# Optimization experiments

Measured on AMD Instinct MI355X. Metric: run time of the kernel, lower is better.

## Reference

```python
import jax, jax.numpy as jnp
import numpy as np

B, S, INPUT_DIM = 8, 512, 64
D_MODEL, NUM_LAYERS, OUTPUT_DIM = 512, 4, 10
D_INNER, D_STATE, D_CONV, DT_RANK = 2 * D_MODEL, 16, 4, 32
GRID_SIZE, SPLINE_K = 5, 3
N_COEFF = GRID_SIZE + SPLINE_K  # 8
_H = 2.0 / GRID_SIZE
GRID = jnp.linspace(-1.0 - SPLINE_K * _H, 1.0 + SPLINE_K * _H, GRID_SIZE + 2 * SPLINE_K + 1)


def b_splines(x):
    # x: (..., in) -> (..., in, N_COEFF) via Cox-de Boor recursion on fixed GRID
    x = x[..., None]
    b = ((x >= GRID[:-1]) & (x < GRID[1:])).astype(x.dtype)
    for p in range(1, SPLINE_K + 1):
        left = (x - GRID[:-(p + 1)]) / (GRID[p:-1] - GRID[:-(p + 1)])
        right = (GRID[p + 1:] - x) / (GRID[p + 1:] - GRID[1:-p])
        b = left * b[..., :-1] + right * b[..., 1:]
    return b


def kan(x, base_w, spline_w):
    # efficient-KAN: silu base path + per-edge spline path
    return jax.nn.silu(x) @ base_w.T + jnp.einsum('...ik,oik->...o', b_splines(x), spline_w)


def layernorm(x, g, b):
    m = jnp.mean(x, -1, keepdims=True)
    v = jnp.var(x, -1, keepdims=True)
    return (x - m) / jnp.sqrt(v + 1e-5) * g + b


def liquid_proj(x, Win, Wrec, b, tau):
    # liquid time-constant RNN: h' = (tanh(Wx + Uh + b) - h) / tau
    pre = x @ Win  # (B,S,H)
    tau_pos = jax.nn.softplus(tau) + 0.1
    def step(h, p):
        act = jnp.tanh(p + h @ Wrec + b)
        h = h + (act - h) / tau_pos
        return h, h
    h0 = jnp.zeros((x.shape[0], Win.shape[1]), x.dtype)
    hT, hs = jax.lax.scan(step, h0, pre.transpose(1, 0, 2))
    return hs.transpose(1, 0, 2), hT


def mamba_block(x, in_proj_w, conv_w, conv_b, x_proj_w, dt_proj_w, dt_proj_b, A_log, Dp, out_proj_w):
    Bb, Ss, _ = x.shape
    xz = x @ in_proj_w.T                       # (B,S,2*di)
    xm, z = jnp.split(xz, 2, axis=-1)
    # causal depthwise conv1d with kernel D_CONV
    xp = jnp.pad(xm, ((0, 0), (D_CONV - 1, 0), (0, 0)))
    xm = sum(xp[:, k:k + Ss, :] * conv_w[:, k] for k in range(D_CONV)) + conv_b
    xm = jax.nn.silu(xm)
    x_dbl = xm @ x_proj_w.T                    # (B,S,dt_rank+2n)
    dt, Bc, Cc = jnp.split(x_dbl, [DT_RANK, DT_RANK + D_STATE], axis=-1)
    dt = jax.nn.softplus(dt @ dt_proj_w.T + dt_proj_b)   # (B,S,di)
    A = -jnp.exp(A_log)                        # (di,n)
    dA = jnp.exp(dt[..., None] * A)            # (B,S,di,n)
    dBu = dt[..., None] * Bc[:, :, None, :] * xm[..., None]
    def step(h, inp):
        a, bu, c = inp
        h = a * h + bu
        return h, jnp.einsum('bdn,bn->bd', h, c)
    h0 = jnp.zeros((Bb, D_INNER, D_STATE), x.dtype)
    _, ys = jax.lax.scan(step, h0, (dA.transpose(1, 0, 2, 3), dBu.transpose(1, 0, 2, 3), Cc.transpose(1, 0, 2)))
    y = ys.transpose(1, 0, 2) + Dp * xm
    y = y * jax.nn.silu(z)
    return y @ out_proj_w.T


def forward(x, lq_Win, lq_Wrec, lq_b, lq_tau, ln_g, ln_b, in_proj_w, conv_w, conv_b,
            x_proj_w, dt_proj_w, dt_proj_b, A_log, Dp, out_proj_w,
            kan_base_w, kan_spline_w, fn_g, fn_b, cls_base_w, cls_spline_w):
    x, _ = liquid_proj(x, lq_Win, lq_Wrec, lq_b, lq_tau)
    for l in range(NUM_LAYERS):
        residual = x
        xn = layernorm(x, ln_g[l], ln_b[l])
        xm = mamba_block(xn, in_proj_w[l], conv_w[l], conv_b[l], x_proj_w[l],
                         dt_proj_w[l], dt_proj_b[l], A_log[l], Dp[l], out_proj_w[l])
        x = residual + kan(xm, kan_base_w[l], kan_spline_w[l])
    x = layernorm(x, fn_g, fn_b)
    return kan(x.mean(axis=1), cls_base_w, cls_spline_w)


def setup_inputs():
    key = jax.random.key(0)
    ks = jax.random.split(key, 12)
    n = lambda k, shape, s: jax.random.normal(k, shape, jnp.float32) * s
    return {
        "x": n(ks[0], (B, S, INPUT_DIM), 1.0),
        "lq_Win": n(ks[1], (INPUT_DIM, D_MODEL), INPUT_DIM ** -0.5),
        "lq_Wrec": n(ks[2], (D_MODEL, D_MODEL), D_MODEL ** -0.5),
        "lq_b": jnp.zeros((D_MODEL,), jnp.float32),
        "lq_tau": jnp.ones((D_MODEL,), jnp.float32),
        "ln_g": jnp.ones((NUM_LAYERS, D_MODEL), jnp.float32),
        "ln_b": jnp.zeros((NUM_LAYERS, D_MODEL), jnp.float32),
        "in_proj_w": n(ks[3], (NUM_LAYERS, 2 * D_INNER, D_MODEL), D_MODEL ** -0.5),
        "conv_w": n(ks[4], (NUM_LAYERS, D_INNER, D_CONV), D_CONV ** -0.5),
        "conv_b": jnp.zeros((NUM_LAYERS, D_INNER), jnp.float32),
        "x_proj_w": n(ks[5], (NUM_LAYERS, DT_RANK + 2 * D_STATE, D_INNER), D_INNER ** -0.5),
        "dt_proj_w": n(ks[6], (NUM_LAYERS, D_INNER, DT_RANK), DT_RANK ** -0.5),
        "dt_proj_b": jnp.full((NUM_LAYERS, D_INNER), float(np.log(np.expm1(0.01))), jnp.float32),
        "A_log": jnp.log(jnp.broadcast_to(jnp.arange(1, D_STATE + 1, dtype=jnp.float32), (NUM_LAYERS, D_INNER, D_STATE))),
        "Dp": jnp.ones((NUM_LAYERS, D_INNER), jnp.float32),
        "out_proj_w": n(ks[7], (NUM_LAYERS, D_MODEL, D_INNER), D_INNER ** -0.5),
        "kan_base_w": n(ks[8], (NUM_LAYERS, D_MODEL, D_MODEL), D_MODEL ** -0.5),
        "kan_spline_w": n(ks[9], (NUM_LAYERS, D_MODEL, D_MODEL, N_COEFF), 0.1 * D_MODEL ** -0.5),
        "fn_g": jnp.ones((D_MODEL,), jnp.float32),
        "fn_b": jnp.zeros((D_MODEL,), jnp.float32),
        "cls_base_w": n(ks[10], (OUTPUT_DIM, D_MODEL), D_MODEL ** -0.5),
        "cls_spline_w": n(ks[11], (OUTPUT_DIM, D_MODEL, N_COEFF), 0.1 * D_MODEL ** -0.5),
    }


def reference(x, lq_Win, lq_Wrec, lq_b, lq_tau, ln_g, ln_b, in_proj_w, conv_w, conv_b,
              x_proj_w, dt_proj_w, dt_proj_b, A_log, Dp, out_proj_w,
              kan_base_w, kan_spline_w, fn_g, fn_b, cls_base_w, cls_spline_w):
    return forward(x, lq_Win, lq_Wrec, lq_b, lq_tau, ln_g, ln_b, in_proj_w, conv_w, conv_b,
                   x_proj_w, dt_proj_w, dt_proj_b, A_log, Dp, out_proj_w,
                   kan_base_w, kan_spline_w, fn_g, fn_b, cls_base_w, cls_spline_w)
```

## Files before the change

### kernel.cpp

```cpp
#include <hip/hip_runtime.h>
#include <hip/hip_bf16.h>
#include <cmath>

#define DEV __device__ __forceinline__

constexpr int B_ = 8, S_ = 512, IN_ = 64, D_ = 512, L_ = 4;
constexpr int DI_ = 1024, DCONV_ = 4, DTR_ = 32;
constexpr int ROWS = B_ * S_;

constexpr size_t MB = 1ull << 20;
constexpr size_t OFF_X    = 0;
constexpr size_t OFF_XN   = OFF_X   + 8*MB;
constexpr size_t OFF_XZ   = OFF_XN  + 8*MB;
constexpr size_t OFF_XM   = OFF_XZ  + 32*MB;
constexpr size_t OFF_DT   = OFF_XM  + 16*MB;
constexpr size_t OFF_XDBL = OFF_DT  + 16*MB;
constexpr size_t OFF_YG   = OFF_XDBL+ 1*MB;
constexpr size_t OFF_MO   = OFF_YG  + 16*MB;
constexpr size_t OFF_WINT = OFF_MO  + 8*MB;
constexpr size_t OFF_MEAN = OFF_WINT+ 128*1024;
constexpr size_t OFF_HBUF = OFF_MEAN+ 16*1024;
constexpr size_t OFF_FLG  = OFF_HBUF+ 32*1024;
constexpr size_t OFF_BASIS= OFF_XZ;

DEV float siluf(float x){ return x / (1.f + __expf(-x)); }
DEV float softplusf(float x){ return fmaxf(x, 0.f) + log1pf(__expf(-fabsf(x))); }
DEV unsigned short f2h(float f){ return __builtin_bit_cast(unsigned short, (_Float16)f); }

DEV void bspline8(float x, float* bb){
  const float h = 0.4f, g0 = -2.2f;
  float b0[11];
#pragma unroll
  for (int j = 0; j < 11; ++j){
    float gj  = g0 + h * j;
    float gj1 = g0 + h * (j + 1);
    b0[j] = (x >= gj && x < gj1) ? 1.f : 0.f;
  }
#pragma unroll
  for (int p = 1; p <= 3; ++p){
    float inv = 1.f / (h * p);
#pragma unroll
    for (int j = 0; j + p < 11; ++j){
      float gj  = g0 + h * j;
      float gip = g0 + h * (j + p + 1);
      b0[j] = (x - gj) * inv * b0[j] + (gip - x) * inv * b0[j + 1];
    }
  }
#pragma unroll
  for (int c = 0; c < 8; ++c) bb[c] = b0[c];
}

template<bool SILU_A, int EPI>
__global__ __launch_bounds__(256)
void gemm_nt(const float* __restrict__ A, int lda,
             const float* __restrict__ W, int ldw,
             float* __restrict__ C, int ldc,
             const float* __restrict__ bias, int K)
{
  __shared__ float As[16][68];
  __shared__ float Ws[16][68];
  const int tid = threadIdx.x;
  const int m0 = blockIdx.y * 64, n0 = blockIdx.x * 64;
  const int lr = tid >> 2, lc = (tid & 3) * 4;
  const float* Ap = A + (size_t)(m0 + lr) * lda + lc;
  const float* Wp = W + (size_t)(n0 + lr) * ldw + lc;
  const int tx = tid & 15, ty = tid >> 4;
  float acc[4][4] = {};
  for (int k0 = 0; k0 < K; k0 += 16){
    float4 a = *(const float4*)(Ap + k0);
    float4 w = *(const float4*)(Wp + k0);
    if (SILU_A){ a.x = siluf(a.x); a.y = siluf(a.y); a.z = siluf(a.z); a.w = siluf(a.w); }
    __syncthreads();
    As[lc+0][lr] = a.x; As[lc+1][lr] = a.y; As[lc+2][lr] = a.z; As[lc+3][lr] = a.w;
    Ws[lc+0][lr] = w.x; Ws[lc+1][lr] = w.y; Ws[lc+2][lr] = w.z; Ws[lc+3][lr] = w.w;
    __syncthreads();
#pragma unroll
    for (int k = 0; k < 16; ++k){
      float4 av = *(const float4*)&As[k][ty*4];
      float4 wv = *(const float4*)&Ws[k][tx*4];
      acc[0][0] += av.x*wv.x; acc[0][1] += av.x*wv.y; acc[0][2] += av.x*wv.z; acc[0][3] += av.x*wv.w;
      acc[1][0] += av.y*wv.x; acc[1][1] += av.y*wv.y; acc[1][2] += av.y*wv.z; acc[1][3] += av.y*wv.w;
      acc[2][0] += av.z*wv.x; acc[2][1] += av.z*wv.y; acc[2][2] += av.z*wv.z; acc[2][3] += av.z*wv.w;
      acc[3][0] += av.w*wv.x; acc[3][1] += av.w*wv.y; acc[3][2] += av.w*wv.z; acc[3][3] += av.w*wv.w;
    }
  }
#pragma unroll
  for (int i = 0; i < 4; ++i){
    float* Crow = C + (size_t)(m0 + ty*4 + i) * ldc + n0 + tx*4;
    float4 r = {acc[i][0], acc[i][1], acc[i][2], acc[i][3]};
    if (EPI == 1){
      float4 c0 = *(const float4*)Crow;
      r.x += c0.x; r.y += c0.y; r.z += c0.z; r.w += c0.w;
    } else if (EPI == 2){
      const float* bp = bias + n0 + tx*4;
      r.x = softplusf(r.x + bp[0]); r.y = softplusf(r.y + bp[1]);
      r.z = softplusf(r.z + bp[2]); r.w = softplusf(r.w + bp[3]);
    }
    *(float4*)Crow = r;
  }
}

typedef _Float16 half8 __attribute__((ext_vector_type(8)));
typedef float f32x4 __attribute__((ext_vector_type(4)));

DEV int pk2(float a, float b){ return (int)((unsigned)f2h(a) | ((unsigned)f2h(b) << 16)); }

template<bool SILU_A, bool ACCUM>
__global__ __launch_bounds__(256)
void gemm_f16(const float* __restrict__ A, int lda,
              const float* __restrict__ W, int ldw,
              float* __restrict__ C, int ldc, int K)
{
  __shared__ unsigned short As[128*40];
  __shared__ unsigned short Bs[128*40];
  const int tid = threadIdx.x;
  const int m0 = blockIdx.y * 128, n0 = blockIdx.x * 128;
  const int wid = tid >> 6, lane = tid & 63;
  const int wm = (wid & 1) * 64, wn = (wid >> 1) * 64;
  const int fr = lane & 15, fk = lane >> 4;
  const int sr = tid >> 1, sh = tid & 1;

  f32x4 acc[4][4];
#pragma unroll
  for (int i = 0; i < 4; ++i)
#pragma unroll
    for (int j = 0; j < 4; ++j)
#pragma unroll
      for (int r = 0; r < 4; ++r) acc[i][j][r] = 0.f;

  for (int k0 = 0; k0 < K; k0 += 32){
    const float* ag = A + (size_t)(m0 + sr) * lda + k0 + sh*16;
    float4 a0 = *(const float4*)ag,     a1 = *(const float4*)(ag+4);
    float4 a2 = *(const float4*)(ag+8), a3 = *(const float4*)(ag+12);
    if (SILU_A){
      a0.x=siluf(a0.x); a0.y=siluf(a0.y); a0.z=siluf(a0.z); a0.w=siluf(a0.w);
      a1.x=siluf(a1.x); a1.y=siluf(a1.y); a1.z=siluf(a1.z); a1.w=siluf(a1.w);
      a2.x=siluf(a2.x); a2.y=siluf(a2.y); a2.z=siluf(a2.z); a2.w=siluf(a2.w);
      a3.x=siluf(a3.x); a3.y=siluf(a3.y); a3.z=siluf(a3.z); a3.w=siluf(a3.w);
    }
    int4 av0 = { pk2(a0.x,a0.y), pk2(a0.z,a0.w), pk2(a1.x,a1.y), pk2(a1.z,a1.w) };
    int4 av1 = { pk2(a2.x,a2.y), pk2(a2.z,a2.w), pk2(a3.x,a3.y), pk2(a3.z,a3.w) };
    const float* wg = W + (size_t)(n0 + sr) * ldw + k0 + sh*16;
    float4 w0 = *(const float4*)wg,     w1 = *(const float4*)(wg+4);
    float4 w2 = *(const float4*)(wg+8), w3 = *(const float4*)(wg+12);
    int4 bv0 = { pk2(w0.x,w0.y), pk2(w0.z,w0.w), pk2(w1.x,w1.y), pk2(w1.z,w1.w) };
    int4 bv1 = { pk2(w2.x,w2.y), pk2(w2.z,w2.w), pk2(w3.x,w3.y), pk2(w3.z,w3.w) };
    __syncthreads();
    *(int4*)&As[sr*40 + sh*16]     = av0;
    *(int4*)&As[sr*40 + sh*16 + 8] = av1;
    *(int4*)&Bs[sr*40 + sh*16]     = bv0;
    *(int4*)&Bs[sr*40 + sh*16 + 8] = bv1;
    __syncthreads();
    half8 a[4], b[4];
#pragma unroll
    for (int i = 0; i < 4; ++i) a[i] = *(const half8*)&As[(wm + i*16 + fr)*40 + fk*8];
#pragma unroll
    for (int j = 0; j < 4; ++j) b[j] = *(const half8*)&Bs[(wn + j*16 + fr)*40 + fk*8];
#pragma unroll
    for (int i = 0; i < 4; ++i)
#pragma unroll
      for (int j = 0; j < 4; ++j)
        acc[i][j] = __builtin_amdgcn_mfma_f32_16x16x32_f16(a[i], b[j], acc[i][j], 0, 0, 0);
  }
#pragma unroll
  for (int i = 0; i < 4; ++i)
#pragma unroll
    for (int j = 0; j < 4; ++j){
      int col = n0 + wn + j*16 + fr;
#pragma unroll
      for (int r = 0; r < 4; ++r){
        int row = m0 + wm + i*16 + fk*4 + r;
        if (ACCUM) C[(size_t)row * ldc + col] += acc[i][j][r];
        else       C[(size_t)row * ldc + col]  = acc[i][j][r];
      }
    }
}

__global__ __launch_bounds__(256)
void gemm_spline_f16(const unsigned short* __restrict__ A,
                     const float* __restrict__ W,
                     float* __restrict__ C)
{
  __shared__ unsigned short As[128*40];
  __shared__ unsigned short Bs[128*40];
  const int tid = threadIdx.x;
  const int m0 = blockIdx.y * 128, n0 = blockIdx.x * 128;
  const int wid = tid >> 6, lane = tid & 63;
  const int wm = (wid & 1) * 64, wn = (wid >> 1) * 64;
  const int fr = lane & 15, fk = lane >> 4;
  const int sr = tid >> 1, sh = tid & 1;

  f32x4 acc[4][4];
#pragma unroll
  for (int i = 0; i < 4; ++i)
#pragma unroll
    for (int j = 0; j < 4; ++j)
#pragma unroll
      for (int r = 0; r < 4; ++r) acc[i][j][r] = 0.f;

  for (int k0 = 0; k0 < 4096; k0 += 32){
    const unsigned short* ag = A + (size_t)(m0 + sr) * 4096 + k0 + sh*16;
    int4 a0 = *(const int4*)ag;
    int4 a1 = *(const int4*)(ag + 8);
    const float* wg = W + (size_t)(n0 + sr) * 4096 + k0 + sh*16;
    float4 w0 = *(const float4*)wg,     w1 = *(const float4*)(wg+4);
    float4 w2 = *(const float4*)(wg+8), w3 = *(const float4*)(wg+12);
    int4 b0 = { pk2(w0.x,w0.y), pk2(w0.z,w0.w), pk2(w1.x,w1.y), pk2(w1.z,w1.w) };
    int4 b1 = { pk2(w2.x,w2.y), pk2(w2.z,w2.w), pk2(w3.x,w3.y), pk2(w3.z,w3.w) };
    __syncthreads();
    *(int4*)&As[sr*40 + sh*16]     = a0;
    *(int4*)&As[sr*40 + sh*16 + 8] = a1;
    *(int4*)&Bs[sr*40 + sh*16]     = b0;
    *(int4*)&Bs[sr*40 + sh*16 + 8] = b1;
    __syncthreads();
    half8 a[4], b[4];
#pragma unroll
    for (int i = 0; i < 4; ++i) a[i] = *(const half8*)&As[(wm + i*16 + fr)*40 + fk*8];
#pragma unroll
    for (int j = 0; j < 4; ++j) b[j] = *(const half8*)&Bs[(wn + j*16 + fr)*40 + fk*8];
#pragma unroll
    for (int i = 0; i < 4; ++i)
#pragma unroll
      for (int j = 0; j < 4; ++j)
        acc[i][j] = __builtin_amdgcn_mfma_f32_16x16x32_f16(a[i], b[j], acc[i][j], 0, 0, 0);
  }
#pragma unroll
  for (int i = 0; i < 4; ++i)
#pragma unroll
    for (int j = 0; j < 4; ++j){
      int col = n0 + wn + j*16 + fr;
#pragma unroll
      for (int r = 0; r < 4; ++r){
        int row = m0 + wm + i*16 + fk*4 + r;
        C[(size_t)row * 512 + col] += acc[i][j][r];
      }
    }
}

__global__ __launch_bounds__(256)
void transpose_win(const float* __restrict__ Win, float* __restrict__ WinT)
{
  int idx = blockIdx.x * 256 + threadIdx.x;
  int n = idx >> 6, k = idx & 63;
  WinT[idx] = Win[(size_t)k * 512 + n];
}

__global__ __launch_bounds__(512)
void liquid_scan3(const float* __restrict__ pre, const float* __restrict__ Wrec,
                  const float* __restrict__ bias, const float* __restrict__ tau,
                  float* __restrict__ xout, float* __restrict__ hbuf,
                  unsigned* __restrict__ flags)
{
  __shared__ float Wl[32800];
  __shared__ float hl[544];
  __shared__ float hnew[64];
  const int tid = threadIdx.x;
  const int bid = blockIdx.x;
  const int slice = bid >> 3, b = bid & 7;
  for (int idx = tid; idx < 512*16; idx += 512){
    int k = idx >> 4, c4 = (idx & 15) * 4;
    float4 w = *(const float4*)(Wrec + (size_t)k*512 + slice*64 + c4);
    *(float4*)&Wl[k*64 + c4 + (k>>6)*4] = w;
  }
  hl[tid + (tid>>6)*4] = 0.f;
  const int o = tid >> 3, kl = tid & 7;
  const int og = slice*64 + o;
  const float tauinv = 1.f / (softplusf(tau[og]) + 0.1f);
  const float bo = bias[og];
  float hold = 0.f;
  const float* preb = pre + (size_t)b * S_ * 512;
  float* xb = xout + (size_t)b * S_ * 512;
  float* hb0 = hbuf + (size_t)b * 512;
  unsigned* bflags = flags + b*8*16;
  unsigned* myflag = bflags + slice*16;
  const int kbase = kl * 64;
  const float* wp = &Wl[(size_t)kbase*64 + o + kl*4];
  __syncthreads();
  for (int t = 0; t < S_; ++t){
    float prev = (kl == 0) ? preb[(size_t)t*512 + og] : 0.f;
    float hreg[64];
#pragma unroll
    for (int j4 = 0; j4 < 16; ++j4)
      *(float4*)&hreg[j4*4] = *(const float4*)&hl[kbase + kl*4 + j4*4];
    float s = 0.f;
#pragma unroll
    for (int j = 0; j < 64; ++j)
      s += hreg[j] * wp[(size_t)j * 64];
    s += __shfl_xor(s, 1);
    s += __shfl_xor(s, 2);
    s += __shfl_xor(s, 4);
    if (kl == 0){
      float act = tanhf(s + prev + bo);
      hold += (act - hold) * tauinv;
      xb[(size_t)t*512 + og] = hold;
      hnew[o] = hold;
    }
    __syncthreads();
    if (tid < 64)
      __hip_atomic_store(hb0 + (t&1)*4096 + slice*64 + tid, hnew[tid],
                         __ATOMIC_RELAXED, __HIP_MEMORY_SCOPE_AGENT);
    if (tid == 0){
      asm volatile("s_waitcnt vmcnt(0)" ::: "memory");
      __hip_atomic_store(myflag, (unsigned)(t+1),
                         __ATOMIC_RELAXED, __HIP_MEMORY_SCOPE_AGENT);
    }
    if (tid < 8){
      while (__hip_atomic_load(bflags + tid*16, __ATOMIC_RELAXED,
                               __HIP_MEMORY_SCOPE_AGENT) < (unsigned)(t+1))
        __builtin_amdgcn_s_sleep(1);
    }
    __syncthreads();
    float hv = __hip_atomic_load(hb0 + (t&1)*4096 + tid,
                                 __ATOMIC_RELAXED, __HIP_MEMORY_SCOPE_AGENT);
    hl[tid + (tid>>6)*4] = hv;
    __syncthreads();
  }
}

__global__ __launch_bounds__(256)
void conv_silu(const float* __restrict__ xz, const float* __restrict__ cw,
               const float* __restrict__ cb, float* __restrict__ xm)
{
  int idx = blockIdx.x * 256 + threadIdx.x;
  int d = idx & 1023;
  int bs = idx >> 10;
  int t = bs & 511;
  const float* p = xz + (size_t)bs * 2048 + d;
  float4 w = *(const float4*)(cw + d*4);
  float acc = cb[d] + w.w * p[0];
  if (t >= 1) acc += w.z * p[-2048];
  if (t >= 2) acc += w.y * p[-2*2048];
  if (t >= 3) acc += w.x * p[-3*2048];
  xm[idx] = siluf(acc);
}

__global__ __launch_bounds__(256)
void mamba_scan(const float* __restrict__ dt, const float* __restrict__ xm,
                const float* __restrict__ xdbl, const float* __restrict__ xz,
                const float* __restrict__ A_log, const float* __restrict__ Dp,
                float* __restrict__ yg)
{
  const int tid = threadIdx.x;
  const int wave = tid >> 6, lane = tid & 63;
  const int half = lane >> 5, dl = lane & 31;
  const int d = blockIdx.x * 128 + wave * 32 + dl;
  const int b = blockIdx.y;
  float A[8];
  {
    float4 a0 = *(const float4*)(A_log + (size_t)d*16 + half*8);
    float4 a1 = *(const float4*)(A_log + (size_t)d*16 + half*8 + 4);
    A[0] = -__expf(a0.x); A[1] = -__expf(a0.y); A[2] = -__expf(a0.z); A[3] = -__expf(a0.w);
    A[4] = -__expf(a1.x); A[5] = -__expf(a1.y); A[6] = -__expf(a1.z); A[7] = -__expf(a1.w);
  }
  const float Dv = Dp[d];
  float h[8] = {0,0,0,0,0,0,0,0};
  const size_t rb = (size_t)b * S_;
  const float* dtp = dt + rb*1024 + d;
  const float* xmp = xm + rb*1024 + d;
  const float* zp  = xz + rb*2048 + 1024 + d;
  const float* bcp = xdbl + rb*64 + 32 + half*8;
  const float* ccp = xdbl + rb*64 + 48 + half*8;
  float* yp = yg + rb*1024 + d;
  for (int t = 0; t < S_; ++t){
    float dtv = dtp[(size_t)t*1024];
    float xv  = xmp[(size_t)t*1024];
    float4 b0 = *(const float4*)(bcp + (size_t)t*64);
    float4 b1 = *(const float4*)(bcp + (size_t)t*64 + 4);
    float4 c0 = *(const float4*)(ccp + (size_t)t*64);
    float4 c1 = *(const float4*)(ccp + (size_t)t*64 + 4);
    float Bv[8] = {b0.x,b0.y,b0.z,b0.w,b1.x,b1.y,b1.z,b1.w};
    float Cv[8] = {c0.x,c0.y,c0.z,c0.w,c1.x,c1.y,c1.z,c1.w};
    float cbu = dtv * xv;
    float y = 0.f;
#pragma unroll
    for (int n = 0; n < 8; ++n){
      float da = __expf(dtv * A[n]);
      h[n] = da * h[n] + cbu * Bv[n];
      y += h[n] * Cv[n];
    }
    y += __shfl_xor(y, 32);
    if (half == 0){
      float zv = zp[(size_t)t*2048];
      yp[(size_t)t*1024] = (y + Dv * xv) * siluf(zv);
    }
  }
}

__global__ __launch_bounds__(256)
void layernorm_k(const float* __restrict__ x, const float* __restrict__ g,
                 const float* __restrict__ b, float* __restrict__ y)
{
  __shared__ float red[8];
  const int row = blockIdx.x, tid = threadIdx.x;
  const float* xr = x + (size_t)row * 512;
  float2 v = *(const float2*)(xr + tid*2);
  float s = v.x + v.y;
#pragma unroll
  for (int o = 32; o; o >>= 1) s += __shfl_xor(s, o);
  if ((tid & 63) == 0) red[tid >> 6] = s;
  __syncthreads();
  float mean = (red[0] + red[1] + red[2] + red[3]) * (1.f/512.f);
  float dx = v.x - mean, dy = v.y - mean;
  float q = dx*dx + dy*dy;
#pragma unroll
  for (int o = 32; o; o >>= 1) q += __shfl_xor(q, o);
  if ((tid & 63) == 0) red[4 + (tid >> 6)] = q;
  __syncthreads();
  float var = (red[4] + red[5] + red[6] + red[7]) * (1.f/512.f);
  float rstd = rsqrtf(var + 1e-5f);
  float2 gg = *(const float2*)(g + tid*2);
  float2 bb = *(const float2*)(b + tid*2);
  float2 o2;
  o2.x = dx*rstd*gg.x + bb.x;
  o2.y = dy*rstd*gg.y + bb.y;
  *(float2*)(y + (size_t)row*512 + tid*2) = o2;
}

__global__ __launch_bounds__(256)
void bspline_kernel(const float* __restrict__ xin, unsigned short* __restrict__ basis)
{
  int idx = blockIdx.x * 256 + threadIdx.x;
  float x = xin[idx];
  float bb[8];
  bspline8(x, bb);
  int4 v = { pk2(bb[0],bb[1]), pk2(bb[2],bb[3]), pk2(bb[4],bb[5]), pk2(bb[6],bb[7]) };
  *(int4*)(basis + (size_t)idx * 8) = v;
}

__global__ __launch_bounds__(512)
void mean_over_s(const float* __restrict__ x, float* __restrict__ out)
{
  int b = blockIdx.x, d = threadIdx.x;
  const float* p = x + (size_t)b*S_*512 + d;
  float s = 0.f;
  for (int t = 0; t < S_; ++t) s += p[(size_t)t*512];
  out[b*512 + d] = s * (1.f/512.f);
}

__global__ __launch_bounds__(64)
void cls_kan(const float* __restrict__ xmean, const float* __restrict__ bw,
             const float* __restrict__ sw, float* __restrict__ out)
{
  int o = blockIdx.x % 10, b = blockIdx.x / 10;
  int lane = threadIdx.x;
  float acc = 0.f;
  for (int i = lane; i < 512; i += 64){
    float xv = xmean[b*512 + i];
    acc += siluf(xv) * bw[o*512 + i];
    float bb[8]; bspline8(xv, bb);
    const float* sp = sw + ((size_t)(o*512 + i)) * 8;
#pragma unroll
    for (int c = 0; c < 8; ++c) acc += bb[c] * sp[c];
  }
#pragma unroll
  for (int off = 32; off; off >>= 1) acc += __shfl_xor(acc, off);
  if (lane == 0) out[b*10 + o] = acc;
}

extern "C" void kernel_launch(void* const* d_in, const int* in_sizes, int n_in,
                              void* d_out, int out_size, void* d_ws, size_t ws_size,
                              hipStream_t stream)
{
  const float* x_in    = (const float*)d_in[0];
  const float* lq_Win  = (const float*)d_in[1];
  const float* lq_Wrec = (const float*)d_in[2];
  const float* lq_b    = (const float*)d_in[3];
  const float* lq_tau  = (const float*)d_in[4];
  const float* ln_g    = (const float*)d_in[5];
  const float* ln_bi   = (const float*)d_in[6];
  const float* in_proj = (const float*)d_in[7];
  const float* conv_w  = (const float*)d_in[8];
  const float* conv_b  = (const float*)d_in[9];
  const float* x_proj  = (const float*)d_in[10];
  const float* dt_w    = (const float*)d_in[11];
  const float* dt_b    = (const float*)d_in[12];
  const float* A_log   = (const float*)d_in[13];
  const float* Dp      = (const float*)d_in[14];
  const float* out_w   = (const float*)d_in[15];
  const float* kb_w    = (const float*)d_in[16];
  const float* ks_w    = (const float*)d_in[17];
  const float* fn_g    = (const float*)d_in[18];
  const float* fn_b    = (const float*)d_in[19];
  const float* cb_w    = (const float*)d_in[20];
  const float* cs_w    = (const float*)d_in[21];
  float* out = (float*)d_out;

  char* ws = (char*)d_ws;
  float* xcur  = (float*)(ws + OFF_X);
  float* xn    = (float*)(ws + OFF_XN);
  float* xz    = (float*)(ws + OFF_XZ);
  float* xm    = (float*)(ws + OFF_XM);
  float* dtb   = (float*)(ws + OFF_DT);
  float* xdbl  = (float*)(ws + OFF_XDBL);
  float* yg    = (float*)(ws + OFF_YG);
  float* mo    = (float*)(ws + OFF_MO);
  float* wint  = (float*)(ws + OFF_WINT);
  float* xmean = (float*)(ws + OFF_MEAN);
  float* hbufp = (float*)(ws + OFF_HBUF);
  unsigned* flgp = (unsigned*)(ws + OFF_FLG);
  unsigned short* basis = (unsigned short*)(ws + OFF_BASIS);

  transpose_win<<<128, 256, 0, stream>>>(lq_Win, wint);
  gemm_nt<false,0><<<dim3(D_/64, ROWS/64), 256, 0, stream>>>(x_in, IN_, wint, IN_, xn, D_, nullptr, IN_);
  hipMemsetAsync(flgp, 0, 8*8*16*sizeof(unsigned), stream);
  liquid_scan3<<<64, 512, 0, stream>>>(xn, lq_Wrec, lq_b, lq_tau, xcur, hbufp, flgp);

  for (int l = 0; l < L_; ++l){
    layernorm_k<<<ROWS, 256, 0, stream>>>(xcur, ln_g + l*D_, ln_bi + l*D_, xn);
    gemm_f16<false,false><<<dim3(2048/128, 4096/128), 256, 0, stream>>>(
        xn, D_, in_proj + (size_t)l*2*DI_*D_, D_, xz, 2*DI_, D_);
    conv_silu<<<ROWS*DI_/256, 256, 0, stream>>>(xz, conv_w + l*DI_*DCONV_, conv_b + l*DI_, xm);
    gemm_nt<false,0><<<dim3(1, ROWS/64), 256, 0, stream>>>(
        xm, DI_, x_proj + (size_t)l*64*DI_, DI_, xdbl, 64, nullptr, DI_);
    gemm_nt<false,2><<<dim3(DI_/64, ROWS/64), 256, 0, stream>>>(
        xdbl, 64, dt_w + (size_t)l*DI_*DTR_, DTR_, dtb, DI_, dt_b + l*DI_, DTR_);
    mamba_scan<<<dim3(DI_/128, B_), 256, 0, stream>>>(
        dtb, xm, xdbl, xz, A_log + (size_t)l*DI_*16, Dp + l*DI_, yg);
    gemm_f16<false,false><<<dim3(512/128, 4096/128), 256, 0, stream>>>(
        yg, DI_, out_w + (size_t)l*D_*DI_, DI_, mo, D_, DI_);
    bspline_kernel<<<ROWS*D_/256, 256, 0, stream>>>(mo, basis);
    gemm_f16<true,true><<<dim3(512/128, 4096/128), 256, 0, stream>>>(
        mo, D_, kb_w + (size_t)l*D_*D_, D_, xcur, D_, D_);
    gemm_spline_f16<<<dim3(512/128, 4096/128), 256, 0, stream>>>(
        basis, ks_w + (size_t)l*D_*D_*8, xcur);
  }

  layernorm_k<<<ROWS, 256, 0, stream>>>(xcur, fn_g, fn_b, xn);
  mean_over_s<<<B_, 512, 0, stream>>>(xn, xmean);
  cls_kan<<<B_*10, 64, 0, stream>>>(xmean, cb_w, cs_w, out);
}
```

Baseline: 4.487 ms.

## Pre-convert weights to fp16, use MFMA for small GEMMs, retile scan and GEMMs

Adds a kernel that converts every layer's weights to fp16 once per call. All GEMMs, including x_proj and dt_proj, now read these fp16 weights and run through MFMA GEMM templates, with a new 128x64 tile variant that gives the N=512 GEMMs more blocks. Layernorm and the Mamba scan now write fp16 activations directly. The scan is reorganised so 8 lanes each hold 2 state elements per channel, which raises parallelism. In exchange there is an extra conversion pass and lower precision for the x_proj and dt_proj paths.

```diff
diff --git a/kernel.cpp b/kernel.cpp
--- a/kernel.cpp
+++ b/kernel.cpp
@@ -21,11 +21,24 @@
 constexpr size_t OFF_MEAN = OFF_WINT+ 128*1024;
 constexpr size_t OFF_HBUF = OFF_MEAN+ 16*1024;
 constexpr size_t OFF_FLG  = OFF_HBUF+ 32*1024;
+constexpr size_t OFF_W16  = OFF_FLG + 64*1024;
 constexpr size_t OFF_BASIS= OFF_XZ;
+
+constexpr size_t W_IP = 0;
+constexpr size_t W_OP = 1048576;
+constexpr size_t W_KB = 1572864;
+constexpr size_t W_KS = 1835008;
+constexpr size_t W_XP = 3932160;
+constexpr size_t W_DT = 3997696;
+constexpr size_t W_PER_LAYER = 4030464;
 
 DEV float siluf(float x){ return x / (1.f + __expf(-x)); }
 DEV float softplusf(float x){ return fmaxf(x, 0.f) + log1pf(__expf(-fabsf(x))); }
 DEV unsigned short f2h(float f){ return __builtin_bit_cast(unsigned short, (_Float16)f); }
+DEV int pk2(float a, float b){ return (int)((unsigned)f2h(a) | ((unsigned)f2h(b) << 16)); }
+
+typedef _Float16 half8 __attribute__((ext_vector_type(8)));
+typedef float f32x4 __attribute__((ext_vector_type(4)));
 
 DEV void bspline8(float x, float* bb){
   const float h = 0.4f, g0 = -2.2f;
@@ -48,6 +61,26 @@
   }
 #pragma unroll
   for (int c = 0; c < 8; ++c) bb[c] = b0[c];
+}
+
+__global__ __launch_bounds__(256)
+void conv_w16(const float* __restrict__ ip, const float* __restrict__ op,
+              const float* __restrict__ kb, const float* __restrict__ ks,
+              const float* __restrict__ xp, const float* __restrict__ dt,
+              unsigned short* __restrict__ w16)
+{
+  int blk = blockIdx.x, tid = threadIdx.x;
+  const float* src; size_t doff; int sb;
+  if      (blk < 512) { src = ip; doff = W_IP; sb = blk; }
+  else if (blk < 768) { src = op; doff = W_OP; sb = blk - 512; }
+  else if (blk < 896) { src = kb; doff = W_KB; sb = blk - 768; }
+  else if (blk < 1920){ src = ks; doff = W_KS; sb = blk - 896; }
+  else if (blk < 1952){ src = xp; doff = W_XP; sb = blk - 1920; }
+  else                { src = dt; doff = W_DT; sb = blk - 1952; }
+  size_t e = (size_t)sb * 2048 + tid * 8;
+  float4 a = *(const float4*)(src + e), b = *(const float4*)(src + e + 4);
+  int4 v = { pk2(a.x,a.y), pk2(a.z,a.w), pk2(b.x,b.y), pk2(b.z,b.w) };
+  *(int4*)&w16[doff + e] = v;
 }
 
 template<bool SILU_A, int EPI>
@@ -88,28 +121,17 @@
   for (int i = 0; i < 4; ++i){
     float* Crow = C + (size_t)(m0 + ty*4 + i) * ldc + n0 + tx*4;
     float4 r = {acc[i][0], acc[i][1], acc[i][2], acc[i][3]};
-    if (EPI == 1){
-      float4 c0 = *(const float4*)Crow;
-      r.x += c0.x; r.y += c0.y; r.z += c0.z; r.w += c0.w;
-    } else if (EPI == 2){
-      const float* bp = bias + n0 + tx*4;
-      r.x = softplusf(r.x + bp[0]); r.y = softplusf(r.y + bp[1]);
-      r.z = softplusf(r.z + bp[2]); r.w = softplusf(r.w + bp[3]);
-    }
     *(float4*)Crow = r;
   }
 }
 
-typedef _Float16 half8 __attribute__((ext_vector_type(8)));
-typedef float f32x4 __attribute__((ext_vector_type(4)));
-
-DEV int pk2(float a, float b){ return (int)((unsigned)f2h(a) | ((unsigned)f2h(b) << 16)); }
-
-template<bool SILU_A, bool ACCUM>
-__global__ __launch_bounds__(256)
-void gemm_f16(const float* __restrict__ A, int lda,
-              const float* __restrict__ W, int ldw,
-              float* __restrict__ C, int ldc, int K)
+
+template<int AMODE, int EPI>
+__global__ __launch_bounds__(256)
+void gemm_h128(const void* __restrict__ Av, int lda,
+               const unsigned short* __restrict__ W,
+               float* __restrict__ C, int ldc,
+               const float* __restrict__ bias, int K)
 {
   __shared__ unsigned short As[128*40];
   __shared__ unsigned short Bs[128*40];
@@ -129,22 +151,25 @@
       for (int r = 0; r < 4; ++r) acc[i][j][r] = 0.f;
 
   for (int k0 = 0; k0 < K; k0 += 32){
-    const float* ag = A + (size_t)(m0 + sr) * lda + k0 + sh*16;
-    float4 a0 = *(const float4*)ag,     a1 = *(const float4*)(ag+4);
-    float4 a2 = *(const float4*)(ag+8), a3 = *(const float4*)(ag+12);
-    if (SILU_A){
-      a0.x=siluf(a0.x); a0.y=siluf(a0.y); a0.z=siluf(a0.z); a0.w=siluf(a0.w);
-      a1.x=siluf(a1.x); a1.y=siluf(a1.y); a1.z=siluf(a1.z); a1.w=siluf(a1.w);
-      a2.x=siluf(a2.x); a2.y=siluf(a2.y); a2.z=siluf(a2.z); a2.w=siluf(a2.w);
-      a3.x=siluf(a3.x); a3.y=siluf(a3.y); a3.z=siluf(a3.z); a3.w=siluf(a3.w);
-    }
-    int4 av0 = { pk2(a0.x,a0.y), pk2(a0.z,a0.w), pk2(a1.x,a1.y), pk2(a1.z,a1.w) };
-    int4 av1 = { pk2(a2.x,a2.y), pk2(a2.z,a2.w), pk2(a3.x,a3.y), pk2(a3.z,a3.w) };
-    const float* wg = W + (size_t)(n0 + sr) * ldw + k0 + sh*16;
-    float4 w0 = *(const float4*)wg,     w1 = *(const float4*)(wg+4);
-    float4 w2 = *(const float4*)(wg+8), w3 = *(const float4*)(wg+12);
-    int4 bv0 = { pk2(w0.x,w0.y), pk2(w0.z,w0.w), pk2(w1.x,w1.y), pk2(w1.z,w1.w) };
-    int4 bv1 = { pk2(w2.x,w2.y), pk2(w2.z,w2.w), pk2(w3.x,w3.y), pk2(w3.z,w3.w) };
+    int4 av0, av1;
+    if (AMODE == 0){
+      const unsigned short* ag = (const unsigned short*)Av + (size_t)(m0 + sr) * lda + k0 + sh*16;
+      av0 = *(const int4*)ag; av1 = *(const int4*)(ag + 8);
+    } else {
+      const float* ag = (const float*)Av + (size_t)(m0 + sr) * lda + k0 + sh*16;
+      float4 a0 = *(const float4*)ag,     a1 = *(const float4*)(ag+4);
+      float4 a2 = *(const float4*)(ag+8), a3 = *(const float4*)(ag+12);
+      if (AMODE == 2){
+        a0.x=siluf(a0.x); a0.y=siluf(a0.y); a0.z=siluf(a0.z); a0.w=siluf(a0.w);
+        a1.x=siluf(a1.x); a1.y=siluf(a1.y); a1.z=siluf(a1.z); a1.w=siluf(a1.w);
+        a2.x=siluf(a2.x); a2.y=siluf(a2.y); a2.z=siluf(a2.z); a2.w=siluf(a2.w);
+        a3.x=siluf(a3.x); a3.y=siluf(a3.y); a3.z=siluf(a3.z); a3.w=siluf(a3.w);
+      }
+      av0 = (int4){ pk2(a0.x,a0.y), pk2(a0.z,a0.w), pk2(a1.x,a1.y), pk2(a1.z,a1.w) };
+      av1 = (int4){ pk2(a2.x,a2.y), pk2(a2.z,a2.w), pk2(a3.x,a3.y), pk2(a3.z,a3.w) };
+    }
+    const unsigned short* wg = W + (size_t)(n0 + sr) * K + k0 + sh*16;
+    int4 bv0 = *(const int4*)wg, bv1 = *(const int4*)(wg + 8);
     __syncthreads();
     *(int4*)&As[sr*40 + sh*16]     = av0;
     *(int4*)&As[sr*40 + sh*16 + 8] = av1;
@@ -170,69 +195,86 @@
 #pragma unroll
       for (int r = 0; r < 4; ++r){
         int row = m0 + wm + i*16 + fk*4 + r;
-        if (ACCUM) C[(size_t)row * ldc + col] += acc[i][j][r];
-        else       C[(size_t)row * ldc + col]  = acc[i][j][r];
+        float* cp = C + (size_t)row * ldc + col;
+        if (EPI == 0)      *cp = acc[i][j][r];
+        else if (EPI == 1) *cp += acc[i][j][r];
+        else               *cp = softplusf(acc[i][j][r] + bias[col]);
       }
     }
 }
 
-__global__ __launch_bounds__(256)
-void gemm_spline_f16(const unsigned short* __restrict__ A,
-                     const float* __restrict__ W,
-                     float* __restrict__ C)
+template<int AMODE, int EPI>
+__global__ __launch_bounds__(256)
+void gemm_h64(const void* __restrict__ Av, int lda,
+              const unsigned short* __restrict__ W,
+              float* __restrict__ C, int ldc,
+              const float* __restrict__ bias, int K)
 {
   __shared__ unsigned short As[128*40];
-  __shared__ unsigned short Bs[128*40];
+  __shared__ unsigned short Bs[64*40];
   const int tid = threadIdx.x;
-  const int m0 = blockIdx.y * 128, n0 = blockIdx.x * 128;
+  const int m0 = blockIdx.y * 128, n0 = blockIdx.x * 64;
   const int wid = tid >> 6, lane = tid & 63;
-  const int wm = (wid & 1) * 64, wn = (wid >> 1) * 64;
   const int fr = lane & 15, fk = lane >> 4;
   const int sr = tid >> 1, sh = tid & 1;
-
-  f32x4 acc[4][4];
-#pragma unroll
-  for (int i = 0; i < 4; ++i)
+  const int br = tid >> 2, bq = tid & 3;
+
+  f32x4 acc[2][4];
+#pragma unroll
+  for (int i = 0; i < 2; ++i)
 #pragma unroll
     for (int j = 0; j < 4; ++j)
 #pragma unroll
       for (int r = 0; r < 4; ++r) acc[i][j][r] = 0.f;
 
-  for (int k0 = 0; k0 < 4096; k0 += 32){
-    const unsigned short* ag = A + (size_t)(m0 + sr) * 4096 + k0 + sh*16;
-    int4 a0 = *(const int4*)ag;
-    int4 a1 = *(const int4*)(ag + 8);
-    const float* wg = W + (size_t)(n0 + sr) * 4096 + k0 + sh*16;
-    float4 w0 = *(const float4*)wg,     w1 = *(const float4*)(wg+4);
-    float4 w2 = *(const float4*)(wg+8), w3 = *(const float4*)(wg+12);
-    int4 b0 = { pk2(w0.x,w0.y), pk2(w0.z,w0.w), pk2(w1.x,w1.y), pk2(w1.z,w1.w) };
-    int4 b1 = { pk2(w2.x,w2.y), pk2(w2.z,w2.w), pk2(w3.x,w3.y), pk2(w3.z,w3.w) };
-    __syncthreads();
-    *(int4*)&As[sr*40 + sh*16]     = a0;
-    *(int4*)&As[sr*40 + sh*16 + 8] = a1;
-    *(int4*)&Bs[sr*40 + sh*16]     = b0;
-    *(int4*)&Bs[sr*40 + sh*16 + 8] = b1;
-    __syncthreads();
-    half8 a[4], b[4];
-#pragma unroll
-    for (int i = 0; i < 4; ++i) a[i] = *(const half8*)&As[(wm + i*16 + fr)*40 + fk*8];
-#pragma unroll
-    for (int j = 0; j < 4; ++j) b[j] = *(const half8*)&Bs[(wn + j*16 + fr)*40 + fk*8];
-#pragma unroll
-    for (int i = 0; i < 4; ++i)
+  for (int k0 = 0; k0 < K; k0 += 32){
+    int4 av0, av1;
+    if (AMODE == 0){
+      const unsigned short* ag = (const unsigned short*)Av + (size_t)(m0 + sr) * lda + k0 + sh*16;
+      av0 = *(const int4*)ag; av1 = *(const int4*)(ag + 8);
+    } else {
+      const float* ag = (const float*)Av + (size_t)(m0 + sr) * lda + k0 + sh*16;
+      float4 a0 = *(const float4*)ag,     a1 = *(const float4*)(ag+4);
+      float4 a2 = *(const float4*)(ag+8), a3 = *(const float4*)(ag+12);
+      if (AMODE == 2){
+        a0.x=siluf(a0.x); a0.y=siluf(a0.y); a0.z=siluf(a0.z); a0.w=siluf(a0.w);
+        a1.x=siluf(a1.x); a1.y=siluf(a1.y); a1.z=siluf(a1.z); a1.w=siluf(a1.w);
+        a2.x=siluf(a2.x); a2.y=siluf(a2.y); a2.z=siluf(a2.z); a2.w=siluf(a2.w);
+        a3.x=siluf(a3.x); a3.y=siluf(a3.y); a3.z=siluf(a3.z); a3.w=siluf(a3.w);
+      }
+      av0 = (int4){ pk2(a0.x,a0.y), pk2(a0.z,a0.w), pk2(a1.x,a1.y), pk2(a1.z,a1.w) };
+      av1 = (int4){ pk2(a2.x,a2.y), pk2(a2.z,a2.w), pk2(a3.x,a3.y), pk2(a3.z,a3.w) };
+    }
+    const unsigned short* wg = W + (size_t)(n0 + br) * K + k0 + bq*8;
+    int4 bv0 = *(const int4*)wg;
+    __syncthreads();
+    *(int4*)&As[sr*40 + sh*16]     = av0;
+    *(int4*)&As[sr*40 + sh*16 + 8] = av1;
+    *(int4*)&Bs[br*40 + bq*8]      = bv0;
+    __syncthreads();
+    half8 a[2], b[4];
+#pragma unroll
+    for (int i = 0; i < 2; ++i) a[i] = *(const half8*)&As[(wid*32 + i*16 + fr)*40 + fk*8];
+#pragma unroll
+    for (int j = 0; j < 4; ++j) b[j] = *(const half8*)&Bs[(j*16 + fr)*40 + fk*8];
+#pragma unroll
+    for (int i = 0; i < 2; ++i)
 #pragma unroll
       for (int j = 0; j < 4; ++j)
         acc[i][j] = __builtin_amdgcn_mfma_f32_16x16x32_f16(a[i], b[j], acc[i][j], 0, 0, 0);
   }
 #pragma unroll
-  for (int i = 0; i < 4; ++i)
+  for (int i = 0; i < 2; ++i)
 #pragma unroll
     for (int j = 0; j < 4; ++j){
-      int col = n0 + wn + j*16 + fr;
+      int col = n0 + j*16 + fr;
 #pragma unroll
       for (int r = 0; r < 4; ++r){
-        int row = m0 + wm + i*16 + fk*4 + r;
-        C[(size_t)row * 512 + col] += acc[i][j][r];
+        int row = m0 + wid*32 + i*16 + fk*4 + r;
+        float* cp = C + (size_t)row * ldc + col;
+        if (EPI == 0)      *cp = acc[i][j][r];
+        else if (EPI == 1) *cp += acc[i][j][r];
+        else               *cp = softplusf(acc[i][j][r] + bias[col]);
       }
     }
 }
@@ -335,60 +377,51 @@
 }
 
 __global__ __launch_bounds__(256)
-void mamba_scan(const float* __restrict__ dt, const float* __restrict__ xm,
-                const float* __restrict__ xdbl, const float* __restrict__ xz,
-                const float* __restrict__ A_log, const float* __restrict__ Dp,
-                float* __restrict__ yg)
+void mamba_scan2(const float* __restrict__ dt, const float* __restrict__ xm,
+                 const float* __restrict__ xdbl, const float* __restrict__ xz,
+                 const float* __restrict__ A_log, const float* __restrict__ Dp,
+                 unsigned short* __restrict__ yg)
 {
   const int tid = threadIdx.x;
   const int wave = tid >> 6, lane = tid & 63;
-  const int half = lane >> 5, dl = lane & 31;
-  const int d = blockIdx.x * 128 + wave * 32 + dl;
+  const int ch = lane >> 3, sub = lane & 7;
+  const int d = blockIdx.x * 32 + wave * 8 + ch;
   const int b = blockIdx.y;
-  float A[8];
-  {
-    float4 a0 = *(const float4*)(A_log + (size_t)d*16 + half*8);
-    float4 a1 = *(const float4*)(A_log + (size_t)d*16 + half*8 + 4);
-    A[0] = -__expf(a0.x); A[1] = -__expf(a0.y); A[2] = -__expf(a0.z); A[3] = -__expf(a0.w);
-    A[4] = -__expf(a1.x); A[5] = -__expf(a1.y); A[6] = -__expf(a1.z); A[7] = -__expf(a1.w);
-  }
+  float2 al = *(const float2*)(A_log + (size_t)d*16 + sub*2);
+  const float A0 = -__expf(al.x), A1 = -__expf(al.y);
   const float Dv = Dp[d];
-  float h[8] = {0,0,0,0,0,0,0,0};
+  float h0 = 0.f, h1 = 0.f;
   const size_t rb = (size_t)b * S_;
   const float* dtp = dt + rb*1024 + d;
   const float* xmp = xm + rb*1024 + d;
   const float* zp  = xz + rb*2048 + 1024 + d;
-  const float* bcp = xdbl + rb*64 + 32 + half*8;
-  const float* ccp = xdbl + rb*64 + 48 + half*8;
-  float* yp = yg + rb*1024 + d;
+  const float* bcp = xdbl + rb*64 + 32 + sub*2;
+  const float* ccp = xdbl + rb*64 + 48 + sub*2;
+  unsigned short* yp = yg + rb*1024 + d;
+#pragma unroll 2
   for (int t = 0; t < S_; ++t){
     float dtv = dtp[(size_t)t*1024];
     float xv  = xmp[(size_t)t*1024];
-    float4 b0 = *(const float4*)(bcp + (size_t)t*64);
-    float4 b1 = *(const float4*)(bcp + (size_t)t*64 + 4);
-    float4 c0 = *(const float4*)(ccp + (size_t)t*64);
-    float4 c1 = *(const float4*)(ccp + (size_t)t*64 + 4);
-    float Bv[8] = {b0.x,b0.y,b0.z,b0.w,b1.x,b1.y,b1.z,b1.w};
-    float Cv[8] = {c0.x,c0.y,c0.z,c0.w,c1.x,c1.y,c1.z,c1.w};
+    float2 B2 = *(const float2*)(bcp + (size_t)t*64);
+    float2 C2 = *(const float2*)(ccp + (size_t)t*64);
     float cbu = dtv * xv;
-    float y = 0.f;
-#pragma unroll
-    for (int n = 0; n < 8; ++n){
-      float da = __expf(dtv * A[n]);
-      h[n] = da * h[n] + cbu * Bv[n];
-      y += h[n] * Cv[n];
-    }
-    y += __shfl_xor(y, 32);
-    if (half == 0){
+    h0 = __expf(dtv * A0) * h0 + cbu * B2.x;
+    h1 = __expf(dtv * A1) * h1 + cbu * B2.y;
+    float y = h0 * C2.x + h1 * C2.y;
+    y += __shfl_xor(y, 1);
+    y += __shfl_xor(y, 2);
+    y += __shfl_xor(y, 4);
+    if (sub == 0){
       float zv = zp[(size_t)t*2048];
-      yp[(size_t)t*1024] = (y + Dv * xv) * siluf(zv);
-    }
-  }
-}
-
+      yp[(size_t)t*1024] = f2h((y + Dv * xv) * siluf(zv));
+    }
+  }
+}
+
+template<bool H>
 __global__ __launch_bounds__(256)
 void layernorm_k(const float* __restrict__ x, const float* __restrict__ g,
-                 const float* __restrict__ b, float* __restrict__ y)
+                 const float* __restrict__ b, void* __restrict__ y)
 {
   __shared__ float red[8];
   const int row = blockIdx.x, tid = threadIdx.x;
@@ -410,10 +443,15 @@
   float rstd = rsqrtf(var + 1e-5f);
   float2 gg = *(const float2*)(g + tid*2);
   float2 bb = *(const float2*)(b + tid*2);
-  float2 o2;
-  o2.x = dx*rstd*gg.x + bb.x;
-  o2.y = dy*rstd*gg.y + bb.y;
-  *(float2*)(y + (size_t)row*512 + tid*2) = o2;
+  float ox = dx*rstd*gg.x + bb.x;
+  float oy = dy*rstd*gg.y + bb.y;
+  if (H){
+    unsigned* yr = (unsigned*)y + (size_t)row*256 + tid;
+    *yr = (unsigned)f2h(ox) | ((unsigned)f2h(oy) << 16);
+  } else {
+    float2 o2 = {ox, oy};
+    *(float2*)((float*)y + (size_t)row*512 + tid*2) = o2;
+  }
 }
 
 __global__ __launch_bounds__(256)
@@ -487,45 +525,56 @@
 
   char* ws = (char*)d_ws;
   float* xcur  = (float*)(ws + OFF_X);
-  float* xn    = (float*)(ws + OFF_XN);
+  float* xn32  = (float*)(ws + OFF_XN);
+  unsigned short* xn16 = (unsigned short*)(ws + OFF_XN);
   float* xz    = (float*)(ws + OFF_XZ);
   float* xm    = (float*)(ws + OFF_XM);
   float* dtb   = (float*)(ws + OFF_DT);
   float* xdbl  = (float*)(ws + OFF_XDBL);
-  float* yg    = (float*)(ws + OFF_YG);
+  unsigned short* yg16 = (unsigned short*)(ws + OFF_YG);
   float* mo    = (float*)(ws + OFF_MO);
   float* wint  = (float*)(ws + OFF_WINT);
   float* xmean = (float*)(ws + OFF_MEAN);
   float* hbufp = (float*)(ws + OFF_HBUF);
   unsigned* flgp = (unsigned*)(ws + OFF_FLG);
+  unsigned short* w16 = (unsigned short*)(ws + OFF_W16);
   unsigned short* basis = (unsigned short*)(ws + OFF_BASIS);
 
   transpose_win<<<128, 256, 0, stream>>>(lq_Win, wint);
-  gemm_nt<false,0><<<dim3(D_/64, ROWS/64), 256, 0, stream>>>(x_in, IN_, wint, IN_, xn, D_, nullptr, IN_);
+  gemm_nt<false,0><<<dim3(D_/64, ROWS/64), 256, 0, stream>>>(x_in, IN_, wint, IN_, xn32, D_, nullptr, IN_);
   hipMemsetAsync(flgp, 0, 8*8*16*sizeof(unsigned), stream);
-  liquid_scan3<<<64, 512, 0, stream>>>(xn, lq_Wrec, lq_b, lq_tau, xcur, hbufp, flgp);
+  liquid_scan3<<<64, 512, 0, stream>>>(xn32, lq_Wrec, lq_b, lq_tau, xcur, hbufp, flgp);
 
   for (int l = 0; l < L_; ++l){
-    layernorm_k<<<ROWS, 256, 0, stream>>>(xcur, ln_g + l*D_, ln_bi + l*D_, xn);
-    gemm_f16<false,false><<<dim3(2048/128, 4096/128), 256, 0, stream>>>(
-        xn, D_, in_proj + (size_t)l*2*DI_*D_, D_, xz, 2*DI_, D_);
+    conv_w16<<<1968, 256, 0, stream>>>(
+        in_proj + (size_t)l*2*DI_*D_, out_w + (size_t)l*D_*DI_,
+        kb_w + (size_t)l*D_*D_, ks_w + (size_t)l*D_*D_*8,
+        x_proj + (size_t)l*64*DI_, dt_w + (size_t)l*DI_*DTR_,
+        w16 + (size_t)l*W_PER_LAYER);
+  }
+
+  for (int l = 0; l < L_; ++l){
+    const unsigned short* wl = w16 + (size_t)l*W_PER_LAYER;
+    layernorm_k<true><<<ROWS, 256, 0, stream>>>(xcur, ln_g + l*D_, ln_bi + l*D_, xn16);
+    gemm_h128<0,0><<<dim3(16, 32), 256, 0, stream>>>(
+        xn16, D_, wl + W_IP, xz, 2*DI_, nullptr, D_);
     conv_silu<<<ROWS*DI_/256, 256, 0, stream>>>(xz, conv_w + l*DI_*DCONV_, conv_b + l*DI_, xm);
-    gemm_nt<false,0><<<dim3(1, ROWS/64), 256, 0, stream>>>(
-        xm, DI_, x_proj + (size_t)l*64*DI_, DI_, xdbl, 64, nullptr, DI_);
-    gemm_nt<false,2><<<dim3(DI_/64, ROWS/64), 256, 0, stream>>>(
-        xdbl, 64, dt_w + (size_t)l*DI_*DTR_, DTR_, dtb, DI_, dt_b + l*DI_, DTR_);
-    mamba_scan<<<dim3(DI_/128, B_), 256, 0, stream>>>(
-        dtb, xm, xdbl, xz, A_log + (size_t)l*DI_*16, Dp + l*DI_, yg);
-    gemm_f16<false,false><<<dim3(512/128, 4096/128), 256, 0, stream>>>(
-        yg, DI_, out_w + (size_t)l*D_*DI_, DI_, mo, D_, DI_);
+    gemm_h64<1,0><<<dim3(1, 32), 256, 0, stream>>>(
+        xm, DI_, wl + W_XP, xdbl, 64, nullptr, DI_);
+    gemm_h128<1,2><<<dim3(8, 32), 256, 0, stream>>>(
+        xdbl, 64, wl + W_DT, dtb, DI_, dt_b + l*DI_, DTR_);
+    mamba_scan2<<<dim3(32, 8), 256, 0, stream>>>(
+        dtb, xm, xdbl, xz, A_log + (size_t)l*DI_*16, Dp + l*DI_, yg16);
+    gemm_h64<0,0><<<dim3(8, 32), 256, 0, stream>>>(
+        yg16, DI_, wl + W_OP, mo, D_, nullptr, DI_);
     bspline_kernel<<<ROWS*D_/256, 256, 0, stream>>>(mo, basis);
-    gemm_f16<true,true><<<dim3(512/128, 4096/128), 256, 0, stream>>>(
-        mo, D_, kb_w + (size_t)l*D_*D_, D_, xcur, D_, D_);
-    gemm_spline_f16<<<dim3(512/128, 4096/128), 256, 0, stream>>>(
-        basis, ks_w + (size_t)l*D_*D_*8, xcur);
-  }
-
-  layernorm_k<<<ROWS, 256, 0, stream>>>(xcur, fn_g, fn_b, xn);
-  mean_over_s<<<B_, 512, 0, stream>>>(xn, xmean);
+    gemm_h64<2,1><<<dim3(8, 32), 256, 0, stream>>>(
+        mo, D_, wl + W_KB, xcur, D_, nullptr, D_);
+    gemm_h64<0,1><<<dim3(8, 32), 256, 0, stream>>>(
+        basis, D_*8, wl + W_KS, xcur, D_, nullptr, D_*8);
+  }
+
+  layernorm_k<false><<<ROWS, 256, 0, stream>>>(xcur, fn_g, fn_b, xn32);
+  mean_over_s<<<B_, 512, 0, stream>>>(xn32, xmean);
   cls_kan<<<B_*10, 64, 0, stream>>>(xmean, cb_w, cs_w, out);
 }
```

New measurement: 3.853 ms. 14.1% less time.
